# Kernel optimization log

Measured on AMD Instinct MI355X. Metric: run time of the kernel, lower is better.

Reference implementation:

```python
import jax, jax.numpy as jnp
import numpy as np

B, T, W, H, F = 256, 128, 32, 512, 1024


def setup_inputs() -> dict:
    key = jax.random.key(0)
    ks = jax.random.split(key, 8)
    s = 0.05
    return {
        "inputs": jax.random.normal(ks[0], (B, T, 2), jnp.float32),
        "Wk": jax.random.normal(ks[1], (2, 4 * H), jnp.float32) * s,
        "Wr": jax.random.normal(ks[2], (H, 4 * H), jnp.float32) * s,
        "b": jnp.zeros((4 * H,), jnp.float32),
        "Ww": jax.random.normal(ks[3], (H, 2), jnp.float32) * s,
        "bw": jnp.zeros((2,), jnp.float32),
        "Wc": jax.random.normal(ks[4], (2, H), jnp.float32) * s,
        "bc": jnp.zeros((H,), jnp.float32),
        "Wcc": jax.random.normal(ks[5], (W * H, F), jnp.float32) * s,
        "bcc": jnp.zeros((F,), jnp.float32),
        "Wp": jax.random.normal(ks[6], (F, 2), jnp.float32) * s,
        "bp": jnp.zeros((2,), jnp.float32),
        "Wco": jax.random.normal(ks[7], (F, 1), jnp.float32) * s,
        "bco": jnp.zeros((1,), jnp.float32),
    }


def _cell(x, h, c, Wk, Wr, b):
    # Keras LSTMCell: gate order i, f, g(candidate), o; sigmoid recurrent act, tanh act.
    z = x @ Wk + h @ Wr + b
    i, f, g, o = jnp.split(z, 4, axis=-1)
    c = jax.nn.sigmoid(f) * c + jax.nn.sigmoid(i) * jnp.tanh(g)
    h = jax.nn.sigmoid(o) * jnp.tanh(c)
    return h, c


def reference(inputs, Wk, Wr, b, Ww, bw, Wc, bc, Wcc, bcc, Wp, bp, Wco, bco):
    # Masking(-1.0) is a no-op for Gaussian inputs; dropout is identity at inference.
    warm_seq = jnp.swapaxes(inputs[:, W:], 0, 1)  # [T-W, B, 2]
    h0 = jnp.zeros((inputs.shape[0], H), inputs.dtype)
    c0 = jnp.zeros_like(h0)

    def warm_step(carry, x):
        h, c = carry
        h, c = _cell(x, h, c, Wk, Wr, b)
        return (h, c), None

    (h, c), _ = jax.lax.scan(warm_step, (h0, c0), warm_seq)
    warm_out = h  # warm_up_lstm_output, [B, H]
    pred0 = h @ Ww + bw  # dense_warm (linear activation), [B, 2]

    def dec_step(carry, _):
        h, c, pred = carry
        h, c = _cell(pred, h, c, Wk, Wr, b)
        pred = h @ Ww + bw
        return (h, c, pred), pred

    n_dec = T - W - 1  # range(1, time - warm_up_length)
    _, preds_rest = jax.lax.scan(dec_step, (h, c, pred0), None, length=n_dec)
    predictions = jnp.concatenate([pred0[None], preds_rest], axis=0)  # [T-W, B, 2]
    predictions = jnp.swapaxes(predictions, 0, 1)  # [B, T-W, 2]

    cand = jax.nn.relu(inputs[:, : W - 1] @ Wc + bc)  # [B, W-1, H]
    cand = cand.reshape(cand.shape[0], -1)  # flatten -> [B, (W-1)*H]
    cat = jnp.concatenate([warm_out, cand], axis=1)  # [B, W*H]
    ct = jax.nn.relu(cat @ Wcc + bcc)  # dense_concat, [B, F]
    candidate_prob = jax.nn.sigmoid(ct @ Wp + bp)  # [B, 2]
    candidate_cost = ct @ Wco + bco  # [B, 1]
    return predictions, candidate_cost, candidate_prob, inputs
```

## Files before the change

kernel.cpp:

```cpp
#include <hip/hip_runtime.h>
#include <hip/hip_bf16.h>
#include <stdint.h>

#define B_    256
#define T_    128
#define W_    32
#define H_    512
#define G4_   2048
#define TW_   96
#define STEPS_ 191
#define TEAMS 16
#define MEMBERS 16
#define ROWS  16
#define HC    32

typedef __attribute__((ext_vector_type(8))) short short8;
typedef __attribute__((ext_vector_type(4))) float f32x4;
typedef __attribute__((ext_vector_type(4))) uint32_t u32x4;

__device__ __forceinline__ unsigned short f2bf(float f) {
  uint32_t u = __float_as_uint(f);
  u += 0x7fffu + ((u >> 16) & 1u);
  return (unsigned short)(u >> 16);
}
__device__ __forceinline__ float sigm(float x) { return 1.f / (1.f + __expf(-x)); }
__device__ __forceinline__ float tanh_(float x) { return 1.f - 2.f / (1.f + __expf(2.f * x)); }

#define LOAD_CF(p)      __hip_atomic_load((p), __ATOMIC_RELAXED, __HIP_MEMORY_SCOPE_AGENT)
#define LOAD_CI(p)      __hip_atomic_load((p), __ATOMIC_RELAXED, __HIP_MEMORY_SCOPE_AGENT)
#define ARRIVE(p)       __hip_atomic_fetch_add((p), 1, __ATOMIC_RELAXED, __HIP_MEMORY_SCOPE_AGENT)

__device__ __forceinline__ u32x4 load_cx4(const void* p) {
  u32x4 v;
  asm volatile("global_load_dwordx4 %0, %1, off sc0 sc1"
               : "=v"(v) : "v"(p) : "memory");
  return v;
}
__device__ __forceinline__ void store_cx4(void* p, u32x4 v) {
  asm volatile("global_store_dwordx4 %0, %1, off sc0 sc1" :: "v"(p), "v"(v) : "memory");
}
__device__ __forceinline__ void store_cfx4(void* p, f32x4 v) {
  asm volatile("global_store_dwordx4 %0, %1, off sc0 sc1" :: "v"(p), "v"(v) : "memory");
}

__global__ __launch_bounds__(256, 1) void lstm_kernel(
    const float* __restrict__ inputs, const float* __restrict__ Wk,
    const float* __restrict__ Wr, const float* __restrict__ bias,
    const float* __restrict__ Ww, const float* __restrict__ bw,
    unsigned short* __restrict__ h0buf, unsigned short* __restrict__ h1buf,
    float* __restrict__ pp0, float* __restrict__ pp1,
    unsigned short* __restrict__ warm, int* __restrict__ flags,
    float* __restrict__ out_pred)
{
  const int team = blockIdx.x & 15;
  const int member = blockIdx.x >> 4;
  const int rbase = team * ROWS;
  const int hbase = member * HC;
  const int tid = threadIdx.x;
  const int wave = tid >> 6;
  const int lane = tid & 63;
  const int l4 = lane >> 4, l16 = lane & 15;

  __shared__ unsigned short h_lds[ROWS][H_];
  __shared__ float x_all_lds[TW_][ROWS][2];
  __shared__ float x_lds[ROWS][2];
  __shared__ float pp_lds[4][ROWS][2];
  __shared__ alignas(16) unsigned short h_out_lds[ROWS][HC];

  for (int i = tid; i < TW_*ROWS*2; i += 256) {
    int tt = i >> 5, row = (i >> 1) & 15, c = i & 1;
    x_all_lds[tt][row][c] = inputs[(size_t)(rbase+row)*(T_*2) + (W_+tt)*2 + c];
  }

  const int gateL = l16 & 3, hclL = l16 >> 2;
  short8 afrag[2][16];
  float bbv[2][4], wk0v[2][4], wk1v[2][4], wwv[2][2];
#pragma unroll
  for (int a = 0; a < 2; a++) {
    const int gcA = gateL*H_ + hbase + wave*8 + a*4 + hclL;
#pragma unroll
    for (int ks = 0; ks < 16; ks++) {
      const float* wp = Wr + (size_t)(ks*32 + l4*8) * G4_ + gcA;
#pragma unroll
      for (int j = 0; j < 8; j++) afrag[a][ks][j] = (short)f2bf(wp[(size_t)j * G4_]);
    }
    const int colA = hbase + wave*8 + a*4 + l4;
#pragma unroll
    for (int j = 0; j < 4; j++) {
      int gcj = j*H_ + colA;
      bbv[a][j] = bias[gcj]; wk0v[a][j] = Wk[gcj]; wk1v[a][j] = Wk[G4_ + gcj];
    }
    wwv[a][0] = Ww[2*colA]; wwv[a][1] = Ww[2*colA + 1];
  }
  const float bwc0 = bw[0], bwc1 = bw[1];
  float creg[2] = {0.f, 0.f};
  __syncthreads();

  int* ctr = flags + team * 16;
  const int srow = tid >> 4, sg = tid & 15;

  for (int t = 0; t < STEPS_; t++) {
    const unsigned short* hprev = (t & 1) ? h1buf : h0buf;
    unsigned short* hnext = (t & 1) ? h0buf : h1buf;
    const float* ppprev = (t & 1) ? pp1 : pp0;
    float* ppnext = (t & 1) ? pp0 : pp1;

    if (t >= TW_ && tid < 32) {
      int row = tid >> 1, c = tid & 1;
      const float* pps = ppprev + (size_t)team*MEMBERS*32 + row*2 + c;
      float s = c ? bwc1 : bwc0;
#pragma unroll
      for (int m = 0; m < MEMBERS; m++) s += LOAD_CF(pps + m*32);
      x_lds[row][c] = s;
      if (member == 0)
        out_pred[((size_t)(rbase+row)*96 + (t - TW_))*2 + c] = s;
    }
    {
      const unsigned short* srcb = hprev + (size_t)(rbase+srow)*H_ + sg*8;
      u32x4 q[4];
#pragma unroll
      for (int i = 0; i < 4; i++) q[i] = load_cx4(srcb + i*128);
      asm volatile("s_waitcnt vmcnt(0)" ::: "memory");
      __builtin_amdgcn_sched_barrier(0);
#pragma unroll
      for (int i = 0; i < 4; i++)
        *(u32x4*)&h_lds[srow][((sg + 16*i) ^ (srow & 7)) * 8] = q[i];
    }
    __syncthreads();

    f32x4 acc[2];
    const float* xsrc = (t < TW_) ? &x_all_lds[t][0][0] : &x_lds[0][0];
    {
      float x0 = xsrc[2*l16], x1 = xsrc[2*l16 + 1];
#pragma unroll
      for (int a = 0; a < 2; a++)
#pragma unroll
        for (int j = 0; j < 4; j++)
          acc[a][j] = bbv[a][j] + wk0v[a][j]*x0 + wk1v[a][j]*x1;
    }
#pragma unroll
    for (int ks = 0; ks < 16; ks++) {
      int pg = ((ks*4 + l4) ^ (l16 & 7)) * 8;
      short8 b0 = *(const short8*)&h_lds[l16][pg];
      acc[0] = __builtin_amdgcn_mfma_f32_16x16x32_bf16(afrag[0][ks], b0, acc[0], 0,0,0);
      acc[1] = __builtin_amdgcn_mfma_f32_16x16x32_bf16(afrag[1][ks], b0, acc[1], 0,0,0);
    }

    float pp0v = 0.f, pp1v = 0.f;
#pragma unroll
    for (int a = 0; a < 2; a++) {
      float zi = acc[a][0], zf = acc[a][1], zg = acc[a][2], zo = acc[a][3];
      float cn = sigm(zf)*creg[a] + sigm(zi)*tanh_(zg);
      float hn = sigm(zo)*tanh_(cn);
      creg[a] = cn;
      pp0v += hn * wwv[a][0];
      pp1v += hn * wwv[a][1];
      h_out_lds[l16][wave*8 + a*4 + l4] = f2bf(hn);
    }
    if (t >= TW_ - 1) {
      pp0v += __shfl_xor(pp0v, 16); pp0v += __shfl_xor(pp0v, 32);
      pp1v += __shfl_xor(pp1v, 16); pp1v += __shfl_xor(pp1v, 32);
      if (l4 == 0) {
        pp_lds[wave][l16][0] = pp0v;
        pp_lds[wave][l16][1] = pp1v;
      }
    }
    __syncthreads();

    if (tid < 64) {
      int row = tid >> 2, q = tid & 3;
      u32x4 v = *(const u32x4*)&h_out_lds[row][q*8];
      store_cx4(hnext + (size_t)(rbase+row)*H_ + hbase + q*8, v);
      if (t == TW_ - 1)
        *(u32x4*)(warm + (size_t)(rbase+row)*H_ + hbase + q*8) = v;
    }
    if (t >= TW_ - 1 && tid < 8) {
      f32x4 pv;
#pragma unroll
      for (int j = 0; j < 4; j++) {
        int idx = tid*4 + j, row = idx >> 1, c = idx & 1;
        pv[j] = pp_lds[0][row][c] + pp_lds[1][row][c]
              + pp_lds[2][row][c] + pp_lds[3][row][c];
      }
      store_cfx4(ppnext + (size_t)(team*MEMBERS + member)*32 + tid*4, pv);
    }

    asm volatile("s_waitcnt vmcnt(0)" ::: "memory");
    __syncthreads();
    if (tid == 0) {
      ARRIVE(ctr);
      int need = MEMBERS * (t + 1);
      while (LOAD_CI(ctr) < need) {}
    }
    __syncthreads();
  }

  if (member == 0 && tid < 32) {
    int row = tid >> 1, c = tid & 1;
    const float* pps = pp1 + (size_t)team*MEMBERS*32 + row*2 + c;
    float s = c ? bwc1 : bwc0;
#pragma unroll
    for (int m = 0; m < MEMBERS; m++) s += LOAD_CF(pps + m*32);
    out_pred[((size_t)(rbase+row)*96 + 95)*2 + c] = s;
  }
}

__global__ void build_cat_kernel(
    const float* __restrict__ inputs, const float* __restrict__ Wc,
    const float* __restrict__ bc, const unsigned short* __restrict__ warm,
    unsigned short* __restrict__ cat)
{
  int idx = (blockIdx.x * 256 + threadIdx.x) * 4;
  int b = idx >> 14, k0 = idx & 16383;
  uint2 out;
  if (k0 < 512) {
    out = *(const uint2*)(warm + (size_t)b*512 + k0);
  } else {
    int kk = k0 - 512;
    int w = kk >> 9;
    int hc = kk & 511;
    float x0 = inputs[(size_t)b*256 + w*2], x1 = inputs[(size_t)b*256 + w*2 + 1];
    unsigned short v[4];
#pragma unroll
    for (int j = 0; j < 4; j++) {
      float val = x0 * Wc[hc+j] + x1 * Wc[512 + hc + j] + bc[hc+j];
      v[j] = f2bf(fmaxf(val, 0.f));
    }
    out.x = (uint32_t)v[0] | ((uint32_t)v[1] << 16);
    out.y = (uint32_t)v[2] | ((uint32_t)v[3] << 16);
  }
  *(uint2*)(cat + idx) = out;
}

__global__ __launch_bounds__(256, 1) void gemm_kernel(
    const unsigned short* __restrict__ cat, const float* __restrict__ Wcc,
    float* __restrict__ partialT)
{
  const int nc = blockIdx.x & 15;
  const int kc = blockIdx.x >> 4;
  const int tid = threadIdx.x;
  const int w = tid >> 6, lane = tid & 63;
  const int l4 = lane >> 4, l16 = lane & 15;

  f32x4 zero = {0.f, 0.f, 0.f, 0.f};
  f32x4 acc[16];
#pragma unroll
  for (int i = 0; i < 16; i++) acc[i] = zero;

  const int kbase = kc * 2048;
  const int nrow = nc*64 + w*16 + l16;

  for (int ks = 0; ks < 64; ks++) {
    const float* wp = Wcc + (size_t)(kbase + ks*32 + l4*8) * 1024 + nrow;
    short8 af;
#pragma unroll
    for (int j = 0; j < 8; j++) af[j] = (short)f2bf(wp[(size_t)j * 1024]);
    const unsigned short* cp = cat + kbase + ks*32 + l4*8;
#pragma unroll
    for (int bt = 0; bt < 16; bt++) {
      short8 bf = *(const short8*)(cp + (size_t)(bt*16 + l16) * 16384);
      acc[bt] = __builtin_amdgcn_mfma_f32_16x16x32_bf16(af, bf, acc[bt], 0, 0, 0);
    }
  }

  float* pp = partialT + (size_t)kc*1024*256 + (size_t)(nc*64 + w*16 + l4*4)*256 + l16;
#pragma unroll
  for (int bt = 0; bt < 16; bt++) {
#pragma unroll
    for (int r = 0; r < 4; r++)
      pp[(size_t)r*256 + bt*16] = acc[bt][r];
  }
}

__global__ void reduce_kernel(const float* __restrict__ partialT,
                              const float* __restrict__ bcc, float* __restrict__ ctT)
{
  int e = blockIdx.x * 256 + threadIdx.x;
  int n = e >> 8;
  float s = bcc[n];
#pragma unroll
  for (int p = 0; p < 8; p++) s += partialT[(size_t)p*262144 + e];
  ctT[e] = fmaxf(s, 0.f);
}

__global__ void head_kernel(const float* __restrict__ ctT, const float* __restrict__ Wp,
                            const float* __restrict__ bp, const float* __restrict__ Wco,
                            const float* __restrict__ bco, float* __restrict__ out)
{
  int b = blockIdx.x;
  int lane = threadIdx.x;
  float p0 = 0.f, p1 = 0.f, pc = 0.f;
#pragma unroll
  for (int i = 0; i < 16; i++) {
    int n = i*64 + lane;
    float c = ctT[(size_t)n*256 + b];
    p0 += c * Wp[2*n]; p1 += c * Wp[2*n+1]; pc += c * Wco[n];
  }
  for (int m = 1; m < 64; m <<= 1) {
    p0 += __shfl_xor(p0, m); p1 += __shfl_xor(p1, m); pc += __shfl_xor(pc, m);
  }
  if (lane == 0) {
    out[49152 + b]       = pc + bco[0];
    out[49408 + 2*b]     = 1.f / (1.f + __expf(-(p0 + bp[0])));
    out[49408 + 2*b + 1] = 1.f / (1.f + __expf(-(p1 + bp[1])));
  }
}

extern "C" void kernel_launch(void* const* d_in, const int* in_sizes, int n_in,
                              void* d_out, int out_size, void* d_ws, size_t ws_size,
                              hipStream_t stream) {
  const float* inputs = (const float*)d_in[0];
  const float* Wk   = (const float*)d_in[1];
  const float* Wr   = (const float*)d_in[2];
  const float* bias = (const float*)d_in[3];
  const float* Ww   = (const float*)d_in[4];
  const float* bw   = (const float*)d_in[5];
  const float* Wc   = (const float*)d_in[6];
  const float* bc   = (const float*)d_in[7];
  const float* Wcc  = (const float*)d_in[8];
  const float* bcc  = (const float*)d_in[9];
  const float* Wp   = (const float*)d_in[10];
  const float* bp   = (const float*)d_in[11];
  const float* Wco  = (const float*)d_in[12];
  const float* bco  = (const float*)d_in[13];
  float* out = (float*)d_out;
  char* ws = (char*)d_ws;

  unsigned short* h0   = (unsigned short*)(ws);
  int*            flags= (int*)(ws + 0x40000);
  unsigned short* h1   = (unsigned short*)(ws + 0x41000);
  unsigned short* warm = (unsigned short*)(ws + 0x81000);
  unsigned short* cat  = (unsigned short*)(ws + 0xC1000);
  float*          pp0  = (float*)(ws + 0xC1000);
  float*          pp1  = (float*)(ws + 0xC9000);
  float*          partialT = (float*)(ws + 0x8C1000);
  float*          ctT  = (float*)(ws + 0x10C1000);

  hipMemsetAsync(d_ws, 0, 0x41000, stream);

  lstm_kernel<<<TEAMS*MEMBERS, 256, 0, stream>>>(inputs, Wk, Wr, bias, Ww, bw,
                                                 h0, h1, pp0, pp1, warm, flags, out);
  build_cat_kernel<<<4096, 256, 0, stream>>>(inputs, Wc, bc, warm, cat);
  gemm_kernel<<<128, 256, 0, stream>>>(cat, Wcc, partialT);
  reduce_kernel<<<1024, 256, 0, stream>>>(partialT, bcc, ctT);
  head_kernel<<<256, 64, 0, stream>>>(ctT, Wp, bp, Wco, bco, out);

  hipMemcpyAsync(out + 49920, inputs, (size_t)65536 * sizeof(float),
                 hipMemcpyDeviceToDevice, stream);
}
```

Measured before the change: 780.0 us.

## Halve LSTM team members to 8 with 512-thread blocks, fold input copy into reduce

```diff
diff --git a/kernel.cpp b/kernel.cpp
--- a/kernel.cpp
+++ b/kernel.cpp
@@ -10,9 +10,9 @@
 #define TW_   96
 #define STEPS_ 191
 #define TEAMS 16
-#define MEMBERS 16
+#define MEMBERS 8
 #define ROWS  16
-#define HC    32
+#define HC    64
 
 typedef __attribute__((ext_vector_type(8))) short short8;
 typedef __attribute__((ext_vector_type(4))) float f32x4;
@@ -30,20 +30,20 @@
 #define LOAD_CI(p)      __hip_atomic_load((p), __ATOMIC_RELAXED, __HIP_MEMORY_SCOPE_AGENT)
 #define ARRIVE(p)       __hip_atomic_fetch_add((p), 1, __ATOMIC_RELAXED, __HIP_MEMORY_SCOPE_AGENT)
 
-__device__ __forceinline__ u32x4 load_cx4(const void* p) {
+__device__ __forceinline__ u32x4 ld16c(const void* p) {
   u32x4 v;
   asm volatile("global_load_dwordx4 %0, %1, off sc0 sc1"
-               : "=v"(v) : "v"(p) : "memory");
+               : "=&v"(v) : "v"(p) : "memory");
   return v;
 }
-__device__ __forceinline__ void store_cx4(void* p, u32x4 v) {
+__device__ __forceinline__ void st16c(void* p, u32x4 v) {
   asm volatile("global_store_dwordx4 %0, %1, off sc0 sc1" :: "v"(p), "v"(v) : "memory");
 }
-__device__ __forceinline__ void store_cfx4(void* p, f32x4 v) {
+__device__ __forceinline__ void stf16c(void* p, f32x4 v) {
   asm volatile("global_store_dwordx4 %0, %1, off sc0 sc1" :: "v"(p), "v"(v) : "memory");
 }
 
-__global__ __launch_bounds__(256, 1) void lstm_kernel(
+__global__ __launch_bounds__(512, 1) void lstm_kernel(
     const float* __restrict__ inputs, const float* __restrict__ Wk,
     const float* __restrict__ Wr, const float* __restrict__ bias,
     const float* __restrict__ Ww, const float* __restrict__ bw,
@@ -62,14 +62,14 @@
   const int l4 = lane >> 4, l16 = lane & 15;
 
   __shared__ unsigned short h_lds[ROWS][H_];
-  __shared__ float x_all_lds[TW_][ROWS][2];
+  __shared__ float x_all[TW_][ROWS][2];
   __shared__ float x_lds[ROWS][2];
-  __shared__ float pp_lds[4][ROWS][2];
-  __shared__ alignas(16) unsigned short h_out_lds[ROWS][HC];
-
-  for (int i = tid; i < TW_*ROWS*2; i += 256) {
+  __shared__ float pp_lds[8][ROWS][2];
+  __shared__ alignas(16) unsigned short h_out[ROWS][HC];
+
+  for (int i = tid; i < TW_*ROWS*2; i += 512) {
     int tt = i >> 5, row = (i >> 1) & 15, c = i & 1;
-    x_all_lds[tt][row][c] = inputs[(size_t)(rbase+row)*(T_*2) + (W_+tt)*2 + c];
+    x_all[tt][row][c] = inputs[(size_t)(rbase+row)*(T_*2) + (W_+tt)*2 + c];
   }
 
   const int gateL = l16 & 3, hclL = l16 >> 2;
@@ -97,7 +97,7 @@
   __syncthreads();
 
   int* ctr = flags + team * 16;
-  const int srow = tid >> 4, sg = tid & 15;
+  const int srow = tid >> 5, sg = tid & 31;
 
   for (int t = 0; t < STEPS_; t++) {
     const unsigned short* hprev = (t & 1) ? h1buf : h0buf;
@@ -105,31 +105,37 @@
     const float* ppprev = (t & 1) ? pp1 : pp0;
     float* ppnext = (t & 1) ? pp0 : pp1;
 
-    if (t >= TW_ && tid < 32) {
+    const bool dox = (t >= TW_) && (tid < 32);
+    float vals[MEMBERS];
+    if (dox) {
       int row = tid >> 1, c = tid & 1;
       const float* pps = ppprev + (size_t)team*MEMBERS*32 + row*2 + c;
+#pragma unroll
+      for (int m = 0; m < MEMBERS; m++) vals[m] = LOAD_CF(pps + m*32);
+    }
+    u32x4 q0, q1;
+    {
+      const unsigned short* srcb = hprev + (size_t)(rbase+srow)*H_ + sg*8;
+      q0 = ld16c(srcb);
+      q1 = ld16c(srcb + 256);
+    }
+    asm volatile("s_waitcnt vmcnt(0)" ::: "memory");
+    __builtin_amdgcn_sched_barrier(0);
+    *(u32x4*)&h_lds[srow][(sg        ^ (srow & 7)) * 8] = q0;
+    *(u32x4*)&h_lds[srow][((sg + 32) ^ (srow & 7)) * 8] = q1;
+    if (dox) {
+      int row = tid >> 1, c = tid & 1;
       float s = c ? bwc1 : bwc0;
 #pragma unroll
-      for (int m = 0; m < MEMBERS; m++) s += LOAD_CF(pps + m*32);
+      for (int m = 0; m < MEMBERS; m++) s += vals[m];
       x_lds[row][c] = s;
       if (member == 0)
         out_pred[((size_t)(rbase+row)*96 + (t - TW_))*2 + c] = s;
     }
-    {
-      const unsigned short* srcb = hprev + (size_t)(rbase+srow)*H_ + sg*8;
-      u32x4 q[4];
-#pragma unroll
-      for (int i = 0; i < 4; i++) q[i] = load_cx4(srcb + i*128);
-      asm volatile("s_waitcnt vmcnt(0)" ::: "memory");
-      __builtin_amdgcn_sched_barrier(0);
-#pragma unroll
-      for (int i = 0; i < 4; i++)
-        *(u32x4*)&h_lds[srow][((sg + 16*i) ^ (srow & 7)) * 8] = q[i];
-    }
     __syncthreads();
 
     f32x4 acc[2];
-    const float* xsrc = (t < TW_) ? &x_all_lds[t][0][0] : &x_lds[0][0];
+    const float* xsrc = (t < TW_) ? &x_all[t][0][0] : &x_lds[0][0];
     {
       float x0 = xsrc[2*l16], x1 = xsrc[2*l16 + 1];
 #pragma unroll
@@ -155,7 +161,7 @@
       creg[a] = cn;
       pp0v += hn * wwv[a][0];
       pp1v += hn * wwv[a][1];
-      h_out_lds[l16][wave*8 + a*4 + l4] = f2bf(hn);
+      h_out[l16][wave*8 + a*4 + l4] = f2bf(hn);
     }
     if (t >= TW_ - 1) {
       pp0v += __shfl_xor(pp0v, 16); pp0v += __shfl_xor(pp0v, 32);
@@ -167,22 +173,24 @@
     }
     __syncthreads();
 
-    if (tid < 64) {
-      int row = tid >> 2, q = tid & 3;
-      u32x4 v = *(const u32x4*)&h_out_lds[row][q*8];
-      store_cx4(hnext + (size_t)(rbase+row)*H_ + hbase + q*8, v);
+    if (tid < 128) {
+      int row = tid >> 3, qd = tid & 7;
+      u32x4 v = *(const u32x4*)&h_out[row][qd*8];
+      st16c(hnext + (size_t)(rbase+row)*H_ + hbase + qd*8, v);
       if (t == TW_ - 1)
-        *(u32x4*)(warm + (size_t)(rbase+row)*H_ + hbase + q*8) = v;
+        *(u32x4*)(warm + (size_t)(rbase+row)*H_ + hbase + qd*8) = v;
     }
     if (t >= TW_ - 1 && tid < 8) {
       f32x4 pv;
 #pragma unroll
       for (int j = 0; j < 4; j++) {
         int idx = tid*4 + j, row = idx >> 1, c = idx & 1;
-        pv[j] = pp_lds[0][row][c] + pp_lds[1][row][c]
-              + pp_lds[2][row][c] + pp_lds[3][row][c];
+        float s = 0.f;
+#pragma unroll
+        for (int w8 = 0; w8 < 8; w8++) s += pp_lds[w8][row][c];
+        pv[j] = s;
       }
-      store_cfx4(ppnext + (size_t)(team*MEMBERS + member)*32 + tid*4, pv);
+      stf16c(ppnext + (size_t)(team*MEMBERS + member)*32 + tid*4, pv);
     }
 
     asm volatile("s_waitcnt vmcnt(0)" ::: "memory");
@@ -273,7 +281,8 @@
 }
 
 __global__ void reduce_kernel(const float* __restrict__ partialT,
-                              const float* __restrict__ bcc, float* __restrict__ ctT)
+                              const float* __restrict__ bcc, float* __restrict__ ctT,
+                              const float* __restrict__ inputs, float* __restrict__ out)
 {
   int e = blockIdx.x * 256 + threadIdx.x;
   int n = e >> 8;
@@ -281,6 +290,7 @@
 #pragma unroll
   for (int p = 0; p < 8; p++) s += partialT[(size_t)p*262144 + e];
   ctT[e] = fmaxf(s, 0.f);
+  if (e < 65536) out[49920 + e] = inputs[e];
 }
 
 __global__ void head_kernel(const float* __restrict__ ctT, const float* __restrict__ Wp,
@@ -328,23 +338,20 @@
 
   unsigned short* h0   = (unsigned short*)(ws);
   int*            flags= (int*)(ws + 0x40000);
-  unsigned short* h1   = (unsigned short*)(ws + 0x41000);
-  unsigned short* warm = (unsigned short*)(ws + 0x81000);
-  unsigned short* cat  = (unsigned short*)(ws + 0xC1000);
-  float*          pp0  = (float*)(ws + 0xC1000);
-  float*          pp1  = (float*)(ws + 0xC9000);
-  float*          partialT = (float*)(ws + 0x8C1000);
-  float*          ctT  = (float*)(ws + 0x10C1000);
-
-  hipMemsetAsync(d_ws, 0, 0x41000, stream);
-
-  lstm_kernel<<<TEAMS*MEMBERS, 256, 0, stream>>>(inputs, Wk, Wr, bias, Ww, bw,
+  unsigned short* h1   = (unsigned short*)(ws + 0x42000);
+  unsigned short* warm = (unsigned short*)(ws + 0x82000);
+  unsigned short* cat  = (unsigned short*)(ws + 0xC2000);
+  float*          pp0  = (float*)(ws + 0xC2000);
+  float*          pp1  = (float*)(ws + 0xC6000);
+  float*          partialT = (float*)(ws + 0x8C2000);
+  float*          ctT  = (float*)(ws + 0x10C2000);
+
+  hipMemsetAsync(d_ws, 0, 0x42000, stream);
+
+  lstm_kernel<<<TEAMS*MEMBERS, 512, 0, stream>>>(inputs, Wk, Wr, bias, Ww, bw,
                                                  h0, h1, pp0, pp1, warm, flags, out);
   build_cat_kernel<<<4096, 256, 0, stream>>>(inputs, Wc, bc, warm, cat);
   gemm_kernel<<<128, 256, 0, stream>>>(cat, Wcc, partialT);
-  reduce_kernel<<<1024, 256, 0, stream>>>(partialT, bcc, ctT);
+  reduce_kernel<<<1024, 256, 0, stream>>>(partialT, bcc, ctT, inputs, out);
   head_kernel<<<256, 64, 0, stream>>>(ctT, Wp, bp, Wco, bco, out);
-
-  hipMemcpyAsync(out + 49920, inputs, (size_t)65536 * sizeof(float),
-                 hipMemcpyDeviceToDevice, stream);
-}
+}
```

Measured after the change: 823.8 us. 1.06x slower.
